# Optimization experiments

Measured on AMD Instinct MI355X. Metric: run time of the kernel, lower is better.

## Reference

```python
import jax, jax.numpy as jnp
import numpy as np

SEP_ID = 102  # bert-base [SEP]


def setup_inputs() -> dict:
    key = jax.random.key(0)
    B, S, H, M = 64, 512, 768, 21
    k1, k2, k3, k4 = jax.random.split(key, 4)
    hidden = jax.random.normal(k1, (B, S, H), dtype=jnp.float32)  # tf1 last_hidden_state
    ids = jax.random.randint(k2, (B, S), 1000, 30000)
    sep_pos = jnp.arange(24, 24 * (M + 1), 24)  # 21 sep positions < 512
    ids = ids.at[:, sep_pos].set(SEP_ID)
    W = jax.random.normal(k3, (H, H), dtype=jnp.float32) * 0.02  # nn.Linear weight [out,in]
    b = jnp.zeros((H,), dtype=jnp.float32)
    v = jax.random.normal(k4, (H,), dtype=jnp.float32) * 0.02    # linear_value [H,1] squeezed
    return {"hidden": hidden, "input_ids": ids, "W": W, "b": b, "v": v,
            "max_sent_count": M}


def _segment_attention_pool(hidden, input_ids, W, b, v, M):
    B, S, H = hidden.shape
    sep = input_ids == SEP_ID                                 # [B,S] bool
    csum = jnp.cumsum(sep.astype(jnp.int32), axis=1)
    seg = csum - sep.astype(jnp.int32)                        # seps strictly before t
    nsep = csum[:, -1]                                        # sentences per row
    pos = jnp.arange(S)
    # sentence k = tokens strictly between sep k-1 and sep k, excluding CLS (pos 0)
    valid = (~sep) & (pos[None, :] >= 1) & (seg < nsep[:, None]) & (seg < M)

    # attention scores: tanh(x @ W.T + b) @ v
    scores = jnp.einsum('bsh,h->bs', jnp.tanh(jnp.einsum('bsh,kh->bsk', hidden, W) + b), v)

    NS = B * M + 1                                            # +1 dummy segment for invalid tokens
    fid = jnp.where(valid, jnp.arange(B)[:, None] * M + seg, B * M).reshape(-1)
    sflat = jnp.where(valid, scores, -jnp.inf).reshape(-1)

    # per-segment stable softmax
    m = jax.ops.segment_max(sflat, fid, num_segments=NS)
    m = jnp.where(jnp.isfinite(m), m, 0.0)                    # empty segments
    e = jnp.where(valid.reshape(-1), jnp.exp(sflat - m[fid]), 0.0)
    denom = jax.ops.segment_sum(e, fid, num_segments=NS)
    w = e / jnp.where(denom[fid] > 0, denom[fid], 1.0)

    sent = jax.ops.segment_sum(w[:, None] * hidden.reshape(-1, H), fid,
                               num_segments=NS)[:B * M].reshape(B, M, H)
    # rows with zero sentences fall back to the CLS embedding (original behavior)
    sent = sent.at[:, 0, :].set(jnp.where((nsep == 0)[:, None], hidden[:, 0, :], sent[:, 0, :]))
    return sent


def reference(hidden, input_ids, W, b, v, max_sent_count):
    return _segment_attention_pool(hidden, input_ids, W, b, v, max_sent_count)
```

## Files before the change

### kernel.cpp

```cpp
#include <hip/hip_runtime.h>


#define SEP_ID 102
#define Bn 64
#define Sn 512
#define Hn 768
#define Mn 21
#define BS (Bn * Sn)

typedef __attribute__((ext_vector_type(8))) short bf16x8;
typedef __attribute__((ext_vector_type(8))) unsigned short u16x8;
typedef __attribute__((ext_vector_type(4))) float f32x4;

__device__ inline unsigned short f2bf(float x) {
  unsigned int u = __builtin_bit_cast(unsigned int, x);
  u += 0x7fffu + ((u >> 16) & 1u);
  return (unsigned short)(u >> 16);
}

__device__ inline u16x8 cvt8v(f32x4 a, f32x4 b) {
  u16x8 r;
  r[0] = f2bf(a[0]); r[1] = f2bf(a[1]); r[2] = f2bf(a[2]); r[3] = f2bf(a[3]);
  r[4] = f2bf(b[0]); r[5] = f2bf(b[1]); r[6] = f2bf(b[2]); r[7] = f2bf(b[3]);
  return r;
}

__device__ inline float tanh_fast(float x) {
  float e = __builtin_amdgcn_exp2f(x * 2.885390081777927f);
  return 1.f - 2.f * __builtin_amdgcn_rcpf(e + 1.f);
}

__global__ void convw_kernel(const float* __restrict__ W, unsigned short* __restrict__ WBp) {
  int c = blockIdx.x * 256 + threadIdx.x;
  int nt = c / 1536;
  int r  = c % 1536;
  int ks = r >> 6;
  int ln = r & 63;
  int col = nt * 16 + (ln & 15);
  int k0  = ks * 32 + (ln >> 4) * 8;
  const f32x4* src = reinterpret_cast<const f32x4*>(&W[col * Hn + k0]);
  f32x4 a = src[0];
  f32x4 b = src[1];
  *reinterpret_cast<u16x8*>(&WBp[(size_t)c * 8]) = cvt8v(a, b);
}

__global__ void segscan_kernel(const int* __restrict__ ids,
                               unsigned char* __restrict__ segv,
                               int* __restrict__ nsep) {
  int b = blockIdx.x;
  int s = threadIdx.x;
  __shared__ int cs[Sn];
  int sep = (ids[b * Sn + s] == SEP_ID) ? 1 : 0;
  cs[s] = sep;
  __syncthreads();
  for (int off = 1; off < Sn; off <<= 1) {
    int add = (s >= off) ? cs[s - off] : 0;
    __syncthreads();
    cs[s] += add;
    __syncthreads();
  }
  int csum = cs[s];
  int nb = cs[Sn - 1];
  int seg = csum - sep;
  bool valid = (!sep) && (s >= 1) && (seg < nb) && (seg < Mn);
  segv[b * Sn + s] = valid ? (unsigned char)seg : (unsigned char)0xFF;
  if (s == 0) nsep[b] = nb;
}

__global__ __launch_bounds__(512, 2) void score_gemm_kernel(
    const float* __restrict__ hid, const unsigned short* __restrict__ WBp,
    const float* __restrict__ bbias, const float* __restrict__ vvec,
    float* __restrict__ scores) {
  __shared__ __align__(16) unsigned short As[64 * 768];
  __shared__ float scpart[8][64];

  const int t = threadIdx.x;
  const size_t rowBase = (size_t)blockIdx.x * 64;
  const int wid = t >> 6, lane = t & 63;
  const int l15 = lane & 15, l4 = lane >> 4;
  const int colBase = wid * 96;

  {
    const int srow = t >> 3;
    const int sq = t & 7;
    const f32x4* hsrc = reinterpret_cast<const f32x4*>(
        &hid[(rowBase + srow) * Hn + sq * 8]);
    unsigned short* const arow = &As[srow * Hn];
    const int wq = (sq ^ (srow & 7));
    f32x4 p[12][2];
#pragma unroll
    for (int j = 0; j < 12; ++j) {
      p[j][0] = hsrc[j * 16];
      p[j][1] = hsrc[j * 16 + 1];
    }
#pragma unroll
    for (int j = 0; j < 12; ++j)
      *reinterpret_cast<u16x8*>(arow + (wq + 8 * j) * 8) = cvt8v(p[j][0], p[j][1]);
  }
  __syncthreads();

  const unsigned short* const afrow = &As[l15 * Hn];
  const int aswz = l15 & 7;
  const unsigned short* bp[6];
#pragma unroll
  for (int ni = 0; ni < 6; ++ni)
    bp[ni] = &WBp[((size_t)(wid * 6 + ni) * 24 * 64 + lane) * 8];

  f32x4 acc[4][6];
#pragma unroll
  for (int mi = 0; mi < 4; ++mi)
#pragma unroll
    for (int ni = 0; ni < 6; ++ni) acc[mi][ni] = (f32x4){0.f, 0.f, 0.f, 0.f};

  bf16x8 afA[4], afB[4], brA[6], brB[6];
#pragma unroll
  for (int mi = 0; mi < 4; ++mi)
    afA[mi] = *reinterpret_cast<const bf16x8*>(
        &afrow[mi * 16 * Hn + ((l4 ^ aswz)) * 8]);
#pragma unroll
  for (int ni = 0; ni < 6; ++ni)
    brA[ni] = *reinterpret_cast<const bf16x8*>(bp[ni]);

#define STEP(kk_, afc, afn, brc, brn)                                       \
  {                                                                         \
    if ((kk_) < 23) {                                                       \
      _Pragma("unroll")                                                     \
      for (int mi = 0; mi < 4; ++mi)                                        \
        afn[mi] = *reinterpret_cast<const bf16x8*>(                         \
            &afrow[mi * 16 * Hn + ((((kk_) + 1) * 4 + l4) ^ aswz) * 8]);    \
      _Pragma("unroll")                                                     \
      for (int ni = 0; ni < 6; ++ni)                                        \
        brn[ni] = *reinterpret_cast<const bf16x8*>(bp[ni] + ((kk_) + 1) * 512); \
    }                                                                       \
    __builtin_amdgcn_sched_barrier(0);                                      \
    _Pragma("unroll")                                                       \
    for (int mi = 0; mi < 4; ++mi)                                          \
      _Pragma("unroll")                                                     \
      for (int ni = 0; ni < 6; ++ni)                                        \
        acc[mi][ni] = __builtin_amdgcn_mfma_f32_16x16x32_bf16(              \
            afc[mi], brc[ni], acc[mi][ni], 0, 0, 0);                        \
  }

#pragma unroll
  for (int k2 = 0; k2 < 12; ++k2) {
    STEP(k2 * 2,     afA, afB, brA, brB)
    STEP(k2 * 2 + 1, afB, afA, brB, brA)
  }
#undef STEP

  float sc[4][4];
#pragma unroll
  for (int mi = 0; mi < 4; ++mi)
#pragma unroll
    for (int r = 0; r < 4; ++r) sc[mi][r] = 0.f;
#pragma unroll
  for (int ni = 0; ni < 6; ++ni) {
    int col = colBase + ni * 16 + l15;
    float vv = vvec[col];
    float bb = bbias[col];
#pragma unroll
    for (int mi = 0; mi < 4; ++mi)
#pragma unroll
      for (int r = 0; r < 4; ++r)
        sc[mi][r] += tanh_fast(acc[mi][ni][r] + bb) * vv;
  }
#pragma unroll
  for (int off = 1; off < 16; off <<= 1)
#pragma unroll
    for (int mi = 0; mi < 4; ++mi)
#pragma unroll
      for (int r = 0; r < 4; ++r)
        sc[mi][r] += __shfl_xor(sc[mi][r], off, 64);
  if (l15 == 0) {
#pragma unroll
    for (int mi = 0; mi < 4; ++mi)
#pragma unroll
      for (int r = 0; r < 4; ++r)
        scpart[wid][mi * 16 + l4 * 4 + r] = sc[mi][r];
  }
  __syncthreads();
  if (t < 64) {
    float s = 0.f;
#pragma unroll
    for (int w = 0; w < 8; ++w) s += scpart[w][t];
    scores[rowBase + t] = s;
  }
}

__global__ __launch_bounds__(256) void pool_kernel(
    const float* __restrict__ hid, const float* __restrict__ scores,
    const unsigned char* __restrict__ segv, const int* __restrict__ nsep,
    float* __restrict__ out) {
  int bm = blockIdx.x;
  int b = bm / Mn, m = bm % Mn;
  int t = threadIdx.x;
  __shared__ float wLds[Sn];
  __shared__ float red[256];
  __shared__ int ired[256];
  const float NEG = -1e30f;

  int base = b * Sn;
  unsigned char mg = (unsigned char)m;
  unsigned char g0 = segv[base + t], g1 = segv[base + 256 + t];
  bool v0 = (g0 == mg), v1 = (g1 == mg);
  float s0 = v0 ? scores[base + t] : NEG;
  float s1 = v1 ? scores[base + 256 + t] : NEG;

  red[t] = fmaxf(s0, s1);
  __syncthreads();
  for (int o = 128; o > 0; o >>= 1) {
    if (t < o) red[t] = fmaxf(red[t], red[t + o]);
    __syncthreads();
  }
  float gmax = red[0];
  __syncthreads();

  size_t obase = (size_t)bm * Hn;
  if (gmax <= -0.5e30f) {
    int nb = nsep[b];
    float a0 = 0.f, a1 = 0.f, a2 = 0.f;
    if (m == 0 && nb == 0) {
      const float* hp = hid + (size_t)base * Hn;
      a0 = hp[t]; a1 = hp[t + 256]; a2 = hp[t + 512];
    }
    out[obase + t] = a0; out[obase + 256 + t] = a1; out[obase + 512 + t] = a2;
    return;
  }

  float e0 = v0 ? expf(s0 - gmax) : 0.f;
  float e1 = v1 ? expf(s1 - gmax) : 0.f;
  red[t] = e0 + e1;
  __syncthreads();
  for (int o = 128; o > 0; o >>= 1) {
    if (t < o) red[t] += red[t + o];
    __syncthreads();
  }
  float inv = 1.f / red[0];
  __syncthreads();
  wLds[t] = e0 * inv;
  wLds[256 + t] = e1 * inv;

  ired[t] = min(v0 ? t : 0x7fffffff, v1 ? (256 + t) : 0x7fffffff);
  __syncthreads();
  for (int o = 128; o > 0; o >>= 1) {
    if (t < o) ired[t] = min(ired[t], ired[t + o]);
    __syncthreads();
  }
  int start = ired[0];
  __syncthreads();
  ired[t] = max(v0 ? t : -1, v1 ? (256 + t) : -1);
  __syncthreads();
  for (int o = 128; o > 0; o >>= 1) {
    if (t < o) ired[t] = max(ired[t], ired[t + o]);
    __syncthreads();
  }
  int end = ired[0];
  __syncthreads();

  float a0 = 0.f, a1 = 0.f, a2 = 0.f;
  for (int s = start; s <= end; ++s) {
    float w = wLds[s];
    if (w != 0.f) {
      const float* hp = hid + (size_t)(base + s) * Hn;
      a0 += w * hp[t];
      a1 += w * hp[t + 256];
      a2 += w * hp[t + 512];
    }
  }
  out[obase + t] = a0;
  out[obase + 256 + t] = a1;
  out[obase + 512 + t] = a2;
}

extern "C" void kernel_launch(void* const* d_in, const int* in_sizes, int n_in,
                              void* d_out, int out_size, void* d_ws, size_t ws_size,
                              hipStream_t stream) {
  const float* hidden = (const float*)d_in[0];
  const int* ids      = (const int*)d_in[1];
  const float* W      = (const float*)d_in[2];
  const float* bbias  = (const float*)d_in[3];
  const float* vvec   = (const float*)d_in[4];

  char* ws = (char*)d_ws;
  unsigned short* WBp  = (unsigned short*)(ws);
  float* scores        = (float*)(ws + 1179648);
  unsigned char* segv  = (unsigned char*)(ws + 1310720);
  int* nsep            = (int*)(ws + 1343488);

  convw_kernel<<<288, 256, 0, stream>>>(W, WBp);
  segscan_kernel<<<Bn, Sn, 0, stream>>>(ids, segv, nsep);
  score_gemm_kernel<<<BS / 64, 512, 0, stream>>>(hidden, WBp, bbias, vvec, scores);
  pool_kernel<<<Bn * Mn, 256, 0, stream>>>(hidden, scores, segv, nsep, (float*)d_out);
}
```

Baseline: 75.78 us.

## Retile score GEMM to 128x384 tiles with LDS-staged B ring and producer warps

The score GEMM now computes 128-row by 384-column tiles per block, splitting the N dimension across two blocks whose partial scores are combined with atomicAdd into a pre-zeroed buffer. Weight fragments are streamed into a three-slot LDS ring via global_load_lds DMA, and the A operand is double-buffered in 128-column K chunks that half the waves prefetch and convert while the others issue MFMAs. This raises reuse of each weight fragment across more rows and overlaps hidden-state loads with compute. The cost is an extra memset, atomics, per-step barriers, and the hidden rows being read by two blocks.

```diff
diff --git a/kernel.cpp b/kernel.cpp
--- a/kernel.cpp
+++ b/kernel.cpp
@@ -28,6 +28,12 @@
 __device__ inline float tanh_fast(float x) {
   float e = __builtin_amdgcn_exp2f(x * 2.885390081777927f);
   return 1.f - 2.f * __builtin_amdgcn_rcpf(e + 1.f);
+}
+
+__device__ inline void dma16(const unsigned short* g, unsigned short* l) {
+  __builtin_amdgcn_global_load_lds(
+      (const __attribute__((address_space(1))) unsigned int*)g,
+      (__attribute__((address_space(3))) unsigned int*)l, 16, 0, 0);
 }
 
 __global__ void convw_kernel(const float* __restrict__ W, unsigned short* __restrict__ WBp) {
@@ -39,9 +45,7 @@
   int col = nt * 16 + (ln & 15);
   int k0  = ks * 32 + (ln >> 4) * 8;
   const f32x4* src = reinterpret_cast<const f32x4*>(&W[col * Hn + k0]);
-  f32x4 a = src[0];
-  f32x4 b = src[1];
-  *reinterpret_cast<u16x8*>(&WBp[(size_t)c * 8]) = cvt8v(a, b);
+  *reinterpret_cast<u16x8*>(&WBp[(size_t)c * 8]) = cvt8v(src[0], src[1]);
 }
 
 __global__ void segscan_kernel(const int* __restrict__ ids,
@@ -71,40 +75,45 @@
     const float* __restrict__ hid, const unsigned short* __restrict__ WBp,
     const float* __restrict__ bbias, const float* __restrict__ vvec,
     float* __restrict__ scores) {
-  __shared__ __align__(16) unsigned short As[64 * 768];
+  __shared__ __align__(16) unsigned short As[2][128 * 128];
+  __shared__ __align__(16) unsigned short Bring[3][24 * 512];
   __shared__ float scpart[8][64];
 
   const int t = threadIdx.x;
-  const size_t rowBase = (size_t)blockIdx.x * 64;
+  const int bid = blockIdx.x;
+  const int bq = bid >> 4, br = bid & 15;
+  const int mIdx = bq * 8 + (br & 7);
+  const int nIdx = br >> 3;
+  const size_t rowBase = (size_t)mIdx * 128;
   const int wid = t >> 6, lane = t & 63;
   const int l15 = lane & 15, l4 = lane >> 4;
-  const int colBase = wid * 96;
+  const int wrow = wid >> 2, wcol = wid & 3;
 
   {
-    const int srow = t >> 3;
-    const int sq = t & 7;
-    const f32x4* hsrc = reinterpret_cast<const f32x4*>(
-        &hid[(rowBase + srow) * Hn + sq * 8]);
-    unsigned short* const arow = &As[srow * Hn];
-    const int wq = (sq ^ (srow & 7));
-    f32x4 p[12][2];
-#pragma unroll
-    for (int j = 0; j < 12; ++j) {
-      p[j][0] = hsrc[j * 16];
-      p[j][1] = hsrc[j * 16 + 1];
-    }
-#pragma unroll
-    for (int j = 0; j < 12; ++j)
-      *reinterpret_cast<u16x8*>(arow + (wq + 8 * j) * 8) = cvt8v(p[j][0], p[j][1]);
-  }
-  __syncthreads();
-
-  const unsigned short* const afrow = &As[l15 * Hn];
-  const int aswz = l15 & 7;
-  const unsigned short* bp[6];
-#pragma unroll
-  for (int ni = 0; ni < 6; ++ni)
-    bp[ni] = &WBp[((size_t)(wid * 6 + ni) * 24 * 64 + lane) * 8];
+    const int row = t >> 2, q4 = t & 3;
+    const f32x4* hs = reinterpret_cast<const f32x4*>(
+        &hid[(rowBase + row) * Hn + q4 * 32]);
+    f32x4 p[8];
+#pragma unroll
+    for (int j = 0; j < 8; ++j) p[j] = hs[j];
+    unsigned short* arow = &As[0][row * 128];
+    const int sw = row & 7;
+#pragma unroll
+    for (int jj = 0; jj < 4; ++jj)
+      *reinterpret_cast<u16x8*>(arow + ((q4 * 4 + jj) ^ sw) * 8) =
+          cvt8v(p[jj * 2], p[jj * 2 + 1]);
+  }
+  if (wid < 4) {
+#pragma unroll
+    for (int s = 0; s < 2; ++s)
+#pragma unroll
+      for (int ni = 0; ni < 6; ++ni) {
+        const int ntg = nIdx * 24 + wcol * 6 + ni;
+        dma16(&WBp[((size_t)(ntg * 24 + s) * 64 + lane) * 8],
+              &Bring[s][(wcol * 6 + ni) * 512]);
+      }
+  }
+  asm volatile("s_waitcnt lgkmcnt(0)" ::: "memory");
 
   f32x4 acc[4][6];
 #pragma unroll
@@ -112,52 +121,72 @@
 #pragma unroll
     for (int ni = 0; ni < 6; ++ni) acc[mi][ni] = (f32x4){0.f, 0.f, 0.f, 0.f};
 
-  bf16x8 afA[4], afB[4], brA[6], brB[6];
+  const int tid2 = t & 255;
+  const int arow2 = tid2 >> 1, ah = tid2 & 1;
+  const int asw2 = arow2 & 7;
+  f32x4 ap[16];
+
+#pragma unroll
+  for (int kk = 0; kk < 24; ++kk) {
+    const int c = kk >> 2, kc = kk & 3, buf = c & 1, slot = kk % 3;
+    if (wid < 4) {
+      if (kk <= 22) asm volatile("s_waitcnt vmcnt(6)" ::: "memory");
+      else          asm volatile("s_waitcnt vmcnt(0)" ::: "memory");
+    }
+    __builtin_amdgcn_s_barrier();
+    __builtin_amdgcn_sched_barrier(0);
+    if (kk + 2 <= 23 && wid < 4) {
+      const int s2 = kk + 2, sl2 = s2 % 3;
+#pragma unroll
+      for (int ni = 0; ni < 6; ++ni) {
+        const int ntg = nIdx * 24 + wcol * 6 + ni;
+        dma16(&WBp[((size_t)(ntg * 24 + s2) * 64 + lane) * 8],
+              &Bring[sl2][(wcol * 6 + ni) * 512]);
+      }
+    }
+    if (kc == 0 && c < 5 && wid >= 4) {
+      const f32x4* hs = reinterpret_cast<const f32x4*>(
+          &hid[(rowBase + arow2) * Hn + (c + 1) * 128 + ah * 64]);
+#pragma unroll
+      for (int j = 0; j < 16; ++j) ap[j] = hs[j];
+    }
+    bf16x8 af[4], bfr[6];
+#pragma unroll
+    for (int mi = 0; mi < 4; ++mi) {
+      const int rw = wrow * 64 + mi * 16 + l15;
+      af[mi] = *reinterpret_cast<const bf16x8*>(
+          &As[buf][rw * 128 + (((kc * 4 + l4) ^ (l15 & 7))) * 8]);
+    }
+#pragma unroll
+    for (int ni = 0; ni < 6; ++ni)
+      bfr[ni] = *reinterpret_cast<const bf16x8*>(
+          &Bring[slot][(wcol * 6 + ni) * 512 + lane * 8]);
+#pragma unroll
+    for (int mi = 0; mi < 4; ++mi)
+#pragma unroll
+      for (int ni = 0; ni < 6; ++ni)
+        acc[mi][ni] = __builtin_amdgcn_mfma_f32_16x16x32_bf16(
+            af[mi], bfr[ni], acc[mi][ni], 0, 0, 0);
+    if (kc == 3 && c < 5 && wid >= 4) {
+      unsigned short* arow = &As[buf ^ 1][arow2 * 128];
+#pragma unroll
+      for (int jj = 0; jj < 8; ++jj)
+        *reinterpret_cast<u16x8*>(arow + ((ah * 8 + jj) ^ asw2) * 8) =
+            cvt8v(ap[jj * 2], ap[jj * 2 + 1]);
+      asm volatile("s_waitcnt lgkmcnt(0)" ::: "memory");
+    }
+  }
+
+  float sc[4][4];
 #pragma unroll
   for (int mi = 0; mi < 4; ++mi)
-    afA[mi] = *reinterpret_cast<const bf16x8*>(
-        &afrow[mi * 16 * Hn + ((l4 ^ aswz)) * 8]);
-#pragma unroll
-  for (int ni = 0; ni < 6; ++ni)
-    brA[ni] = *reinterpret_cast<const bf16x8*>(bp[ni]);
-
-#define STEP(kk_, afc, afn, brc, brn)                                       \
-  {                                                                         \
-    if ((kk_) < 23) {                                                       \
-      _Pragma("unroll")                                                     \
-      for (int mi = 0; mi < 4; ++mi)                                        \
-        afn[mi] = *reinterpret_cast<const bf16x8*>(                         \
-            &afrow[mi * 16 * Hn + ((((kk_) + 1) * 4 + l4) ^ aswz) * 8]);    \
-      _Pragma("unroll")                                                     \
-      for (int ni = 0; ni < 6; ++ni)                                        \
-        brn[ni] = *reinterpret_cast<const bf16x8*>(bp[ni] + ((kk_) + 1) * 512); \
-    }                                                                       \
-    __builtin_amdgcn_sched_barrier(0);                                      \
-    _Pragma("unroll")                                                       \
-    for (int mi = 0; mi < 4; ++mi)                                          \
-      _Pragma("unroll")                                                     \
-      for (int ni = 0; ni < 6; ++ni)                                        \
-        acc[mi][ni] = __builtin_amdgcn_mfma_f32_16x16x32_bf16(              \
-            afc[mi], brc[ni], acc[mi][ni], 0, 0, 0);                        \
-  }
-
-#pragma unroll
-  for (int k2 = 0; k2 < 12; ++k2) {
-    STEP(k2 * 2,     afA, afB, brA, brB)
-    STEP(k2 * 2 + 1, afB, afA, brB, brA)
-  }
-#undef STEP
-
-  float sc[4][4];
-#pragma unroll
-  for (int mi = 0; mi < 4; ++mi)
 #pragma unroll
     for (int r = 0; r < 4; ++r) sc[mi][r] = 0.f;
 #pragma unroll
   for (int ni = 0; ni < 6; ++ni) {
-    int col = colBase + ni * 16 + l15;
-    float vv = vvec[col];
-    float bb = bbias[col];
+    const int col = nIdx * 384 + wcol * 96 + ni * 16 + l15;
+    const float vv = vvec[col];
+    const float bb = bbias[col];
 #pragma unroll
     for (int mi = 0; mi < 4; ++mi)
 #pragma unroll
@@ -179,11 +208,11 @@
         scpart[wid][mi * 16 + l4 * 4 + r] = sc[mi][r];
   }
   __syncthreads();
-  if (t < 64) {
+  if (t < 128) {
     float s = 0.f;
 #pragma unroll
-    for (int w = 0; w < 8; ++w) s += scpart[w][t];
-    scores[rowBase + t] = s;
+    for (int wc = 0; wc < 4; ++wc) s += scpart[(t >> 6) * 4 + wc][t & 63];
+    atomicAdd(&scores[rowBase + t], s);
   }
 }
 
@@ -289,6 +318,7 @@
 
   convw_kernel<<<288, 256, 0, stream>>>(W, WBp);
   segscan_kernel<<<Bn, Sn, 0, stream>>>(ids, segv, nsep);
-  score_gemm_kernel<<<BS / 64, 512, 0, stream>>>(hidden, WBp, bbias, vvec, scores);
+  hipMemsetAsync(scores, 0, BS * sizeof(float), stream);
+  score_gemm_kernel<<<512, 512, 0, stream>>>(hidden, WBp, bbias, vvec, scores);
   pool_kernel<<<Bn * Mn, 256, 0, stream>>>(hidden, scores, segv, nsep, (float*)d_out);
 }
```

After: 90.60 us. 1.2x slower.

## Switch score GEMM from 16x16x32 to 32x32x16 bf16 MFMA tiles

Applied to the files above, without the earlier changes.

Replaces the 16x16x32 MFMA tiling in the score GEMM with 32x32x16 MFMAs, using 2x3 accumulator tiles of 16 floats per wave. The weight pre-pack layout and the LDS A-fragment addressing change to match. The epilogue reduction and row mapping are adapted to the 32x32 output layout. The aim is fewer MFMA issues and fewer fragment loads per FLOP, at the cost of more accumulator registers, a longer cross-lane reduction, and a possible change in LDS bank-conflict behaviour from the new swizzle use.

```diff
diff --git a/kernel.cpp b/kernel.cpp
--- a/kernel.cpp
+++ b/kernel.cpp
@@ -11,6 +11,7 @@
 typedef __attribute__((ext_vector_type(8))) short bf16x8;
 typedef __attribute__((ext_vector_type(8))) unsigned short u16x8;
 typedef __attribute__((ext_vector_type(4))) float f32x4;
+typedef __attribute__((ext_vector_type(16))) float f32x16;
 
 __device__ inline unsigned short f2bf(float x) {
   unsigned int u = __builtin_bit_cast(unsigned int, x);
@@ -32,12 +33,12 @@
 
 __global__ void convw_kernel(const float* __restrict__ W, unsigned short* __restrict__ WBp) {
   int c = blockIdx.x * 256 + threadIdx.x;
-  int nt = c / 1536;
-  int r  = c % 1536;
-  int ks = r >> 6;
+  int nt = c / 3072;
+  int r  = c % 3072;
+  int kc = r >> 6;
   int ln = r & 63;
-  int col = nt * 16 + (ln & 15);
-  int k0  = ks * 32 + (ln >> 4) * 8;
+  int col = nt * 32 + (ln & 31);
+  int k0  = kc * 16 + (ln >> 5) * 8;
   const f32x4* src = reinterpret_cast<const f32x4*>(&W[col * Hn + k0]);
   f32x4 a = src[0];
   f32x4 b = src[1];
@@ -77,7 +78,7 @@
   const int t = threadIdx.x;
   const size_t rowBase = (size_t)blockIdx.x * 64;
   const int wid = t >> 6, lane = t & 63;
-  const int l15 = lane & 15, l4 = lane >> 4;
+  const int l31 = lane & 31, l5 = lane >> 5;
   const int colBase = wid * 96;
 
   {
@@ -99,46 +100,60 @@
   }
   __syncthreads();
 
-  const unsigned short* const afrow = &As[l15 * Hn];
-  const int aswz = l15 & 7;
-  const unsigned short* bp[6];
-#pragma unroll
-  for (int ni = 0; ni < 6; ++ni)
-    bp[ni] = &WBp[((size_t)(wid * 6 + ni) * 24 * 64 + lane) * 8];
-
-  f32x4 acc[4][6];
-#pragma unroll
-  for (int mi = 0; mi < 4; ++mi)
-#pragma unroll
-    for (int ni = 0; ni < 6; ++ni) acc[mi][ni] = (f32x4){0.f, 0.f, 0.f, 0.f};
+  const unsigned short* const afrow = &As[l31 * Hn];
+  const int aswz = lane & 7;
+  const unsigned short* bp[3];
+#pragma unroll
+  for (int ni = 0; ni < 3; ++ni)
+    bp[ni] = &WBp[((size_t)(wid * 3 + ni) * 48 * 64 + lane) * 8];
+
+  f32x16 acc[2][3];
+#pragma unroll
+  for (int mi = 0; mi < 2; ++mi)
+#pragma unroll
+    for (int ni = 0; ni < 3; ++ni)
+#pragma unroll
+      for (int r = 0; r < 16; ++r) acc[mi][ni][r] = 0.f;
 
   bf16x8 afA[4], afB[4], brA[6], brB[6];
 #pragma unroll
-  for (int mi = 0; mi < 4; ++mi)
-    afA[mi] = *reinterpret_cast<const bf16x8*>(
-        &afrow[mi * 16 * Hn + ((l4 ^ aswz)) * 8]);
-#pragma unroll
-  for (int ni = 0; ni < 6; ++ni)
-    brA[ni] = *reinterpret_cast<const bf16x8*>(bp[ni]);
-
-#define STEP(kk_, afc, afn, brc, brn)                                       \
-  {                                                                         \
-    if ((kk_) < 23) {                                                       \
-      _Pragma("unroll")                                                     \
-      for (int mi = 0; mi < 4; ++mi)                                        \
-        afn[mi] = *reinterpret_cast<const bf16x8*>(                         \
-            &afrow[mi * 16 * Hn + ((((kk_) + 1) * 4 + l4) ^ aswz) * 8]);    \
-      _Pragma("unroll")                                                     \
-      for (int ni = 0; ni < 6; ++ni)                                        \
-        brn[ni] = *reinterpret_cast<const bf16x8*>(bp[ni] + ((kk_) + 1) * 512); \
-    }                                                                       \
-    __builtin_amdgcn_sched_barrier(0);                                      \
-    _Pragma("unroll")                                                       \
-    for (int mi = 0; mi < 4; ++mi)                                          \
-      _Pragma("unroll")                                                     \
-      for (int ni = 0; ni < 6; ++ni)                                        \
-        acc[mi][ni] = __builtin_amdgcn_mfma_f32_16x16x32_bf16(              \
-            afc[mi], brc[ni], acc[mi][ni], 0, 0, 0);                        \
+  for (int mi = 0; mi < 2; ++mi)
+#pragma unroll
+    for (int h = 0; h < 2; ++h)
+      afA[mi * 2 + h] = *reinterpret_cast<const bf16x8*>(
+          &afrow[mi * 32 * Hn + ((h * 2 + l5) ^ aswz) * 8]);
+#pragma unroll
+  for (int ni = 0; ni < 3; ++ni)
+#pragma unroll
+    for (int h = 0; h < 2; ++h)
+      brA[ni * 2 + h] = *reinterpret_cast<const bf16x8*>(bp[ni] + h * 512);
+
+#define STEP(kk_, afc, afn, brc, brn)                                        \
+  {                                                                          \
+    if ((kk_) < 23) {                                                        \
+      _Pragma("unroll")                                                      \
+      for (int mi = 0; mi < 2; ++mi)                                         \
+        _Pragma("unroll")                                                    \
+        for (int h = 0; h < 2; ++h)                                          \
+          afn[mi * 2 + h] = *reinterpret_cast<const bf16x8*>(                \
+              &afrow[mi * 32 * Hn +                                          \
+                     ((((kk_) + 1) * 4 + h * 2 + l5) ^ aswz) * 8]);          \
+      _Pragma("unroll")                                                      \
+      for (int ni = 0; ni < 3; ++ni)                                         \
+        _Pragma("unroll")                                                    \
+        for (int h = 0; h < 2; ++h)                                          \
+          brn[ni * 2 + h] = *reinterpret_cast<const bf16x8*>(                \
+              bp[ni] + (((kk_) + 1) * 2 + h) * 512);                         \
+    }                                                                        \
+    __builtin_amdgcn_sched_barrier(0);                                       \
+    _Pragma("unroll")                                                        \
+    for (int mi = 0; mi < 2; ++mi)                                           \
+      _Pragma("unroll")                                                      \
+      for (int ni = 0; ni < 3; ++ni)                                         \
+        _Pragma("unroll")                                                    \
+        for (int h = 0; h < 2; ++h)                                          \
+          acc[mi][ni] = __builtin_amdgcn_mfma_f32_32x32x16_bf16(             \
+              afc[mi * 2 + h], brc[ni * 2 + h], acc[mi][ni], 0, 0, 0);       \
   }
 
 #pragma unroll
@@ -148,35 +163,37 @@
   }
 #undef STEP
 
-  float sc[4][4];
-#pragma unroll
-  for (int mi = 0; mi < 4; ++mi)
-#pragma unroll
-    for (int r = 0; r < 4; ++r) sc[mi][r] = 0.f;
-#pragma unroll
-  for (int ni = 0; ni < 6; ++ni) {
-    int col = colBase + ni * 16 + l15;
-    float vv = vvec[col];
-    float bb = bbias[col];
-#pragma unroll
-    for (int mi = 0; mi < 4; ++mi)
-#pragma unroll
-      for (int r = 0; r < 4; ++r)
+  float sc[2][16];
+#pragma unroll
+  for (int mi = 0; mi < 2; ++mi)
+#pragma unroll
+    for (int r = 0; r < 16; ++r) sc[mi][r] = 0.f;
+#pragma unroll
+  for (int ni = 0; ni < 3; ++ni) {
+    const int col = colBase + ni * 32 + l31;
+    const float vv = vvec[col];
+    const float bb = bbias[col];
+#pragma unroll
+    for (int mi = 0; mi < 2; ++mi)
+#pragma unroll
+      for (int r = 0; r < 16; ++r)
         sc[mi][r] += tanh_fast(acc[mi][ni][r] + bb) * vv;
   }
 #pragma unroll
-  for (int off = 1; off < 16; off <<= 1)
-#pragma unroll
-    for (int mi = 0; mi < 4; ++mi)
-#pragma unroll
-      for (int r = 0; r < 4; ++r)
+  for (int off = 1; off < 32; off <<= 1)
+#pragma unroll
+    for (int mi = 0; mi < 2; ++mi)
+#pragma unroll
+      for (int r = 0; r < 16; ++r)
         sc[mi][r] += __shfl_xor(sc[mi][r], off, 64);
-  if (l15 == 0) {
-#pragma unroll
-    for (int mi = 0; mi < 4; ++mi)
-#pragma unroll
-      for (int r = 0; r < 4; ++r)
-        scpart[wid][mi * 16 + l4 * 4 + r] = sc[mi][r];
+  if (l31 == 0) {
+#pragma unroll
+    for (int mi = 0; mi < 2; ++mi)
+#pragma unroll
+      for (int r = 0; r < 16; ++r) {
+        const int rowL = mi * 32 + (r & 3) + 8 * (r >> 2) + 4 * l5;
+        scpart[wid][rowL] = sc[mi][r];
+      }
   }
   __syncthreads();
   if (t < 64) {
```

New measurement: 81.74 us. 7.9% more time.
